# Kernel optimization log

Measured on AMD Instinct MI355X. Metric: run time of the kernel, lower is better.

The kernel has to match this reference:

```python
import jax, jax.numpy as jnp
import numpy as np

HEADS = 16
NUM_LANDMARKS = 64
PINV_ITERS = 6
D_MODEL = 1024


def _moore_penrose_pinv(x, num_iters):
    # Newton-Schulz iteration: V <- 0.25*V @ (13I - KV @ (15I - KV @ (7I - KV)))
    m = x.shape[-1]
    I = jnp.eye(m, dtype=x.dtype)
    V = x
    for _ in range(num_iters):
        KV = x @ V  # [..., m, m]
        V = 0.25 * V @ (13.0 * I - KV @ (15.0 * I - KV @ (7.0 * I - KV)))
    return V


def setup_inputs() -> dict:
    key = jax.random.key(0)
    k1, k2, k3 = jax.random.split(key, 3)
    b, n, d = 4, 4096, D_MODEL
    hidden_states = jax.random.normal(k1, (b, n, d), dtype=jnp.float32)
    Wqkv = jax.random.normal(k2, (d, 3 * d), dtype=jnp.float32) * 0.02
    bqkv = jnp.zeros((3 * d,), dtype=jnp.float32)
    Wout = jax.random.normal(k3, (d, d), dtype=jnp.float32) * 0.02
    bout = jnp.zeros((d,), dtype=jnp.float32)
    return {"hidden_states": hidden_states, "Wqkv": Wqkv, "bqkv": bqkv,
            "Wout": Wout, "bout": bout}


def reference(hidden_states, Wqkv, bqkv, Wout, bout):
    b, n, d = hidden_states.shape
    h, m = HEADS, NUM_LANDMARKS
    dh = d // h
    scale = 1.0 / np.sqrt(dh).astype(np.float32)
    # n is a multiple of m by construction, so the torch padding branch is a no-op.
    l = n // m  # tokens per landmark group

    qkv = hidden_states @ Wqkv + bqkv  # [b, n, 3d]
    q, k, v = jnp.split(qkv, 3, axis=-1)

    def to_heads(t):  # [b, n, d] -> [b, h, n, dh]
        return t.reshape(b, n, h, dh).transpose(0, 2, 1, 3)

    q, k, v = to_heads(q), to_heads(k), to_heads(v)
    q = q * scale

    # Landmarks: mean over contiguous groups of l tokens (sum / l in original).
    q_l = q.reshape(b, h, m, l, dh).mean(axis=3)  # [b, h, m, dh]
    k_l = k.reshape(b, h, m, l, dh).mean(axis=3)

    sim1 = jnp.einsum('bhid,bhjd->bhij', q, k_l)    # [b, h, n, m]
    sim2 = jnp.einsum('bhid,bhjd->bhij', q_l, k_l)  # [b, h, m, m]
    sim3 = jnp.einsum('bhid,bhjd->bhij', q_l, k)    # [b, h, m, n]

    attn1 = jax.nn.softmax(sim1, axis=-1)
    attn2 = jax.nn.softmax(sim2, axis=-1)
    attn3 = jax.nn.softmax(sim3, axis=-1)

    attn2_inv = _moore_penrose_pinv(attn2, PINV_ITERS)

    # out = attn1 @ attn2_inv @ (attn3 @ v), cheapest association
    out = attn1 @ (attn2_inv @ (attn3 @ v))  # [b, h, n, dh]
    out = out.transpose(0, 2, 1, 3).reshape(b, n, d)
    out = out @ Wout + bout
    return out
```

## Files before the change

### kernel.cpp

```cpp
#include <hip/hip_runtime.h>
#include <cstdint>

typedef unsigned short u16;
typedef __attribute__((ext_vector_type(8))) short s16x8;
typedef __attribute__((ext_vector_type(4))) float f32x4;

#define NTOK 4096
#define DH   64
#define DM   1024
#define NH   16

static __device__ __forceinline__ float b2f(u16 u){ return __uint_as_float(((unsigned)u)<<16); }
static __device__ __forceinline__ u16 f2b(float f){
  unsigned u = __float_as_uint(f);
  return (u16)((u + 0x7FFFu + ((u>>16)&1u)) >> 16);
}

static __device__ __forceinline__ void gload_lds16(const void* g, void* l) {
  __builtin_amdgcn_global_load_lds(
      (const __attribute__((address_space(1))) unsigned*)(uintptr_t)g,
      (__attribute__((address_space(3))) unsigned*)(uintptr_t)l, 16, 0, 0);
}

static __device__ __forceinline__ s16x8 ld8(const u16* p){ return *(const s16x8*)(const void*)p; }

__global__ __launch_bounds__(256) void k_cvt(const float* __restrict__ in, u16* __restrict__ out, long n4) {
  long i = (long)blockIdx.x*blockDim.x + threadIdx.x;
  const long st = (long)gridDim.x*blockDim.x;
  for (; i < n4; i += st) {
    const float4 v = ((const float4*)in)[i];
    ushort4 o; o.x=f2b(v.x); o.y=f2b(v.y); o.z=f2b(v.z); o.w=f2b(v.w);
    ((ushort4*)out)[i] = o;
  }
}

__global__ __launch_bounds__(256) void k_cvt_t(const float* __restrict__ in, u16* __restrict__ out, int R, int C) {
  __shared__ float tile[64][65];
  const int tc = blockIdx.x, tr = blockIdx.y;
  const int t = threadIdx.x, cx = t & 63, ry = t >> 6;
  #pragma unroll
  for (int p = 0; p < 16; ++p) {
    const int row = p*4 + ry;
    tile[row][cx] = in[(long)(tr*64 + row)*C + tc*64 + cx];
  }
  __syncthreads();
  #pragma unroll
  for (int p = 0; p < 16; ++p) {
    const int orow = p*4 + ry;
    out[(long)(tc*64 + orow)*R + tr*64 + cx] = f2b(tile[cx][orow]);
  }
}

__global__ __launch_bounds__(256) void k_xlmean(const float* __restrict__ hs, float* __restrict__ Xl) {
  const int row = blockIdx.x;
  const int b = row >> 6, lm = row & 63;
  const int d = blockIdx.y*256 + threadIdx.x;
  const float* p = hs + ((long)b*NTOK + lm*64)*DM + d;
  float s = 0.f;
  #pragma unroll 16
  for (int i = 0; i < 64; ++i) s += p[(long)i*DM];
  Xl[(long)row*DM + d] = s * (1.0f/64.0f);
}

__global__ __launch_bounds__(256) void k_lproj2(const float* __restrict__ Xl, const float* __restrict__ Wqkv,
                                                float* __restrict__ psum) {
  __shared__ __align__(16) float Xs[32][68];
  const int t = threadIdx.x;
  const int wcol = blockIdx.x*256 + t;
  const int r0 = blockIdx.y*32;
  const int kbase = blockIdx.z*128;
  float acc[32];
  #pragma unroll
  for (int r = 0; r < 32; ++r) acc[r] = 0.f;
  for (int k0 = kbase; k0 < kbase + 128; k0 += 64) {
    __syncthreads();
    for (int idx = t; idx < 2048; idx += 256)
      Xs[idx>>6][idx&63] = Xl[(long)(r0 + (idx>>6))*DM + k0 + (idx&63)];
    __syncthreads();
    for (int kk = 0; kk < 64; kk += 4) {
      f32x4 wv;
      #pragma unroll
      for (int j = 0; j < 4; ++j) wv[j] = Wqkv[(long)(k0+kk+j)*3072 + wcol];
      #pragma unroll
      for (int r = 0; r < 32; ++r) {
        const f32x4 xv = *(const f32x4*)&Xs[r][kk];
        acc[r] += xv[0]*wv[0] + xv[1]*wv[1] + xv[2]*wv[2] + xv[3]*wv[3];
      }
    }
  }
  float* po = psum + ((long)blockIdx.z*256 + r0)*2048 + wcol;
  #pragma unroll
  for (int r = 0; r < 32; ++r) po[(long)r*2048] = acc[r];
}

__global__ __launch_bounds__(256) void k_lreduce(const float* __restrict__ psum, const float* __restrict__ bqkv,
                                                 float* __restrict__ qlf, float* __restrict__ klf,
                                                 u16* __restrict__ qlb, u16* __restrict__ klb) {
  const long idx = (long)blockIdx.x*256 + threadIdx.x;
  const int row = (int)(idx >> 11), col = (int)(idx & 2047);
  float s = 0.f;
  #pragma unroll
  for (int z = 0; z < 8; ++z) s += psum[((long)z*256 + row)*2048 + col];
  const int isq = (col < 1024) ? 1 : 0;
  float val = s + bqkv[col];
  if (isq) val *= 0.125f;
  const int b = row >> 6, lm = row & 63;
  const int c2 = col & 1023, h = c2 >> 6, dh = c2 & 63;
  const long o = (((long)b*NH + h)*64 + lm)*64 + dh;
  if (isq) { qlf[o] = val; qlb[o] = f2b(val); }
  else     { klf[o] = val; klb[o] = f2b(val); }
}

template<int EPI>
__global__ __launch_bounds__(512, 2) void k_gemm256(
    const u16* __restrict__ A, const u16* __restrict__ Bt, const float* __restrict__ bias,
    int N, float* __restrict__ outF, u16* __restrict__ outQ, u16* __restrict__ outK, u16* __restrict__ outV)
{
  __shared__ __align__(16) u16 lds[4*16384];
  const int K = 1024;
  const int t = threadIdx.x;
  const int lane = t & 63;
  const int wid = t >> 6;
  const int c = lane & 15, g = lane >> 4;
  const int wm = wid >> 2, wn = wid & 3;
  const long arow0 = (long)blockIdx.x * 256;
  const long brow0 = (long)blockIdx.y * 256;
  char* ldsb = (char*)lds;

  const int srow = t >> 2;
  const int schunk = (t & 3) ^ ((srow >> 1) & 3);
  const u16* gA0 = A  + (arow0 + srow)*K       + schunk*8;
  const u16* gA1 = A  + (arow0 + 128 + srow)*K + schunk*8;
  const u16* gB0 = Bt + (brow0 + srow)*K       + schunk*8;
  const u16* gB1 = Bt + (brow0 + 128 + srow)*K + schunk*8;
  const int dstoff = t*16;

#define STAGE_A(kt) { char* bse = ldsb + ((kt)&3)*32768; \
    gload_lds16(gA0 + (kt)*32, bse + dstoff); \
    gload_lds16(gA1 + (kt)*32, bse + 8192 + dstoff); }
#define STAGE_B(kt) { char* bse = ldsb + ((kt)&3)*32768 + 16384; \
    gload_lds16(gB0 + (kt)*32, bse + dstoff); \
    gload_lds16(gB1 + (kt)*32, bse + 8192 + dstoff); }

  const int gs = g ^ ((c >> 1) & 3);
  int aoff[2][4], boff[4];
  #pragma unroll
  for (int mi = 0; mi < 4; ++mi) {
    aoff[0][mi] = (0*128 + wm*64 + mi*16 + c)*64 + gs*16;
    aoff[1][mi] = (1*128 + wm*64 + mi*16 + c)*64 + gs*16;
    boff[mi]    = 16384 + (wn*64 + mi*16 + c)*64 + gs*16;
  }

  f32x4 acc0[4][4] = {};
  f32x4 acc1[4][4] = {};

  STAGE_A(0); STAGE_B(0); STAGE_A(1); STAGE_B(1); STAGE_A(2); STAGE_B(2);
  asm volatile("s_waitcnt vmcnt(8)" ::: "memory");
  __builtin_amdgcn_s_barrier();

  for (int kt = 0; kt < 32; ++kt) {
    char* buf = ldsb + (kt&3)*32768;
    if (kt + 3 < 32) { STAGE_A(kt+3) STAGE_B(kt+3) }
    s16x8 af[4], af2[4], bfr[4];
    #pragma unroll
    for (int mi = 0; mi < 4; ++mi) af[mi]  = *(const s16x8*)(buf + aoff[0][mi]);
    #pragma unroll
    for (int ni = 0; ni < 4; ++ni) bfr[ni] = *(const s16x8*)(buf + boff[ni]);
    #pragma unroll
    for (int mi = 0; mi < 4; ++mi) af2[mi] = *(const s16x8*)(buf + aoff[1][mi]);
    asm volatile("s_waitcnt lgkmcnt(0)" ::: "memory");
    __builtin_amdgcn_sched_barrier(0);
    __builtin_amdgcn_s_setprio(1);
    #pragma unroll
    for (int mi = 0; mi < 4; ++mi)
      #pragma unroll
      for (int ni = 0; ni < 4; ++ni)
        acc0[mi][ni] = __builtin_amdgcn_mfma_f32_16x16x32_bf16(af[mi], bfr[ni], acc0[mi][ni], 0, 0, 0);
    #pragma unroll
    for (int mi = 0; mi < 4; ++mi)
      #pragma unroll
      for (int ni = 0; ni < 4; ++ni)
        acc1[mi][ni] = __builtin_amdgcn_mfma_f32_16x16x32_bf16(af2[mi], bfr[ni], acc1[mi][ni], 0, 0, 0);
    __builtin_amdgcn_s_setprio(0);
    if (kt <= 28)      { asm volatile("s_waitcnt vmcnt(8)" ::: "memory"); }
    else if (kt == 29) { asm volatile("s_waitcnt vmcnt(4)" ::: "memory"); }
    else if (kt == 30) { asm volatile("s_waitcnt vmcnt(0)" ::: "memory"); }
    __builtin_amdgcn_s_barrier();
  }
#undef STAGE_A
#undef STAGE_B

  if (EPI == 0) {
    const int tensor = (int)(brow0 >> 10);
    u16* dst = (tensor == 0) ? outQ : (tensor == 1) ? outK : outV;
    const float mul = (tensor == 0) ? 0.125f : 1.0f;
    #pragma unroll
    for (int ph = 0; ph < 2; ++ph)
      #pragma unroll
      for (int mi = 0; mi < 4; ++mi) {
        const int rowb = ph*128 + wm*64 + mi*16 + g*4;
        #pragma unroll
        for (int ni = 0; ni < 4; ++ni) {
          const long gcol = brow0 + wn*64 + ni*16 + c;
          const int c2 = (int)(gcol & 1023);
          const int head = c2 >> 6, dh = c2 & 63;
          const float bv = bias[gcol];
          const f32x4 a = ph ? acc1[mi][ni] : acc0[mi][ni];
          #pragma unroll
          for (int r = 0; r < 4; ++r) {
            const long grow = arow0 + rowb + r;
            const int b = (int)(grow >> 12), tok = (int)(grow & 4095);
            dst[(((long)b*NH + head)*NTOK + tok)*DH + dh] = f2b((a[r] + bv)*mul);
          }
        }
      }
  } else {
    #pragma unroll
    for (int ph = 0; ph < 2; ++ph)
      #pragma unroll
      for (int mi = 0; mi < 4; ++mi) {
        const int rowb = ph*128 + wm*64 + mi*16 + g*4;
        #pragma unroll
        for (int ni = 0; ni < 4; ++ni) {
          const long gcol = brow0 + wn*64 + ni*16 + c;
          const float bv = bias[gcol];
          const f32x4 a = ph ? acc1[mi][ni] : acc0[mi][ni];
          #pragma unroll
          for (int r = 0; r < 4; ++r) {
            const long grow = arow0 + rowb + r;
            outF[grow*N + gcol] = a[r] + bv;
          }
        }
      }
  }
}

__global__ __launch_bounds__(256) void k_vtrans(const u16* __restrict__ v, u16* __restrict__ vt) {
  __shared__ u16 tile[64][65];
  const int bh = blockIdx.x >> 6, tt = blockIdx.x & 63;
  const int t = threadIdx.x, cx = t & 63, ry = t >> 6;
  const u16* vp = v + ((long)bh*NTOK + tt*64)*DH;
  #pragma unroll
  for (int p = 0; p < 16; ++p) { const int row = p*4 + ry; tile[row][cx] = vp[row*DH + cx]; }
  __syncthreads();
  u16* op = vt + (long)bh*DH*NTOK + tt*64;
  #pragma unroll
  for (int p = 0; p < 16; ++p) { const int orow = p*4 + ry; op[(long)orow*NTOK + cx] = tile[cx][orow]; }
}

#define PST 68
static __device__ __forceinline__ void mm_nn8(const float* A, const float* B, float* C, int t) {
  const int lane = t & 63, j0 = (t >> 6) << 3;
  float acc[8];
  #pragma unroll
  for (int j = 0; j < 8; ++j) acc[j] = 0.f;
  for (int k = 0; k < 64; k += 4) {
    const f32x4 a4 = *(const f32x4*)&A[lane*PST + k];
    #pragma unroll
    for (int dk = 0; dk < 4; ++dk) {
      const float a = a4[dk];
      const float* br = &B[(k + dk)*PST + j0];
      const f32x4 b0 = *(const f32x4*)(br);
      const f32x4 b1 = *(const f32x4*)(br + 4);
      #pragma unroll
      for (int qq = 0; qq < 4; ++qq) { acc[qq] += a*b0[qq]; acc[4+qq] += a*b1[qq]; }
    }
  }
  #pragma unroll
  for (int j = 0; j < 8; ++j) C[lane*PST + j0 + j] = acc[j];
}
static __device__ __forceinline__ void mm_nt8(const float* A, const float* B, float* C, int t) {
  const int lane = t & 63, j0 = (t >> 6) << 3;
  float acc[8];
  #pragma unroll
  for (int j = 0; j < 8; ++j) acc[j] = 0.f;
  for (int k = 0; k < 64; k += 4) {
    const f32x4 a4 = *(const f32x4*)&A[lane*PST + k];
    #pragma unroll
    for (int jj = 0; jj < 8; ++jj) {
      const f32x4 b4 = *(const f32x4*)&B[(j0 + jj)*PST + k];
      acc[jj] += a4[0]*b4[0] + a4[1]*b4[1] + a4[2]*b4[2] + a4[3]*b4[3];
    }
  }
  #pragma unroll
  for (int j = 0; j < 8; ++j) C[lane*PST + j0 + j] = acc[j];
}

__global__ __launch_bounds__(512) void k_pinv(const float* __restrict__ qlf, const float* __restrict__ klf,
                                              float* __restrict__ a2inv) {
  __shared__ __align__(16) float Xb[64*PST];
  __shared__ __align__(16) float Vb[64*PST];
  __shared__ __align__(16) float T1[64*PST];
  __shared__ __align__(16) float T2[64*PST];
  __shared__ __align__(16) float T3[64*PST];
  const int bh = blockIdx.x, t = threadIdx.x;
  const float* ql = qlf + (long)bh*4096;
  const float* kl = klf + (long)bh*4096;
  for (int i = t; i < 4096; i += 512) { T1[(i>>6)*PST + (i&63)] = ql[i]; T2[(i>>6)*PST + (i&63)] = kl[i]; }
  __syncthreads();
  mm_nt8(T1, T2, Xb, t);
  __syncthreads();
  if (t < 64) {
    float mx = -1e30f;
    for (int j = 0; j < 64; ++j) mx = fmaxf(mx, Xb[t*PST + j]);
    float s = 0.f;
    for (int j = 0; j < 64; ++j) { const float e = expf(Xb[t*PST + j] - mx); Xb[t*PST + j] = e; s += e; }
    const float inv = 1.0f/s;
    for (int j = 0; j < 64; ++j) Xb[t*PST + j] *= inv;
  }
  __syncthreads();
  for (int i = t; i < 4096; i += 512) { const int r = i>>6, cc = i&63; Vb[r*PST+cc] = Xb[r*PST+cc]; }
  __syncthreads();
  for (int it = 0; it < 6; ++it) {
    mm_nn8(Xb, Vb, T1, t);  __syncthreads();
    for (int i = t; i < 4096; i += 512) { const int r=i>>6, cc=i&63; T2[r*PST+cc] = (r==cc?7.0f:0.0f) - T1[r*PST+cc]; }
    __syncthreads();
    mm_nn8(T1, T2, T3, t);  __syncthreads();
    for (int i = t; i < 4096; i += 512) { const int r=i>>6, cc=i&63; T2[r*PST+cc] = (r==cc?15.0f:0.0f) - T3[r*PST+cc]; }
    __syncthreads();
    mm_nn8(T1, T2, T3, t);  __syncthreads();
    for (int i = t; i < 4096; i += 512) { const int r=i>>6, cc=i&63; T2[r*PST+cc] = (r==cc?13.0f:0.0f) - T3[r*PST+cc]; }
    __syncthreads();
    mm_nn8(Vb, T2, T3, t);  __syncthreads();
    for (int i = t; i < 4096; i += 512) { const int r=i>>6, cc=i&63; Vb[r*PST+cc] = 0.25f*T3[r*PST+cc]; }
    __syncthreads();
  }
  for (int i = t; i < 4096; i += 512) a2inv[(long)bh*4096 + i] = Vb[(i>>6)*PST + (i&63)];
}

__global__ __launch_bounds__(256) void k_attn3v_p(const u16* __restrict__ qlb, const u16* __restrict__ kk,
                                                  const u16* __restrict__ vt,
                                                  float* __restrict__ zp, float* __restrict__ sp) {
  __shared__ __align__(16) float Zl[4][64][64];
  __shared__ float Sl[4][64];
  __shared__ __align__(16) u16 Pl[4][64][40];
  const int bh = blockIdx.x >> 2, qt = blockIdx.x & 3;
  const int t = threadIdx.x, w = t >> 6, lane = t & 63;
  const int c = lane & 15, g = lane >> 4;

  s16x8 aq[4][2];
  const u16* qlp = qlb + (long)bh*4096;
  #pragma unroll
  for (int mi = 0; mi < 4; ++mi)
    #pragma unroll
    for (int ks = 0; ks < 2; ++ks)
      aq[mi][ks] = ld8(qlp + (mi*16 + c)*64 + ks*32 + g*8);

  f32x4 zacc[4][4] = {};
  float sl[4][4] = {};
  const u16* kp = kk + (long)bh*NTOK*DH;
  const u16* vp = vt + (long)bh*DH*NTOK;
  char* pbase = (char*)&Pl[w][0][0];
  const int tok00 = qt*1024 + w*256;

  for (int it = 0; it < 8; ++it) {
    const int t0 = tok00 + it*32;
    f32x4 sacc[4][2] = {};
    s16x8 kb[2][2];
    #pragma unroll
    for (int cg = 0; cg < 2; ++cg)
      #pragma unroll
      for (int ks = 0; ks < 2; ++ks)
        kb[cg][ks] = ld8(kp + (long)(t0 + cg*16 + c)*64 + ks*32 + g*8);
    #pragma unroll
    for (int cg = 0; cg < 2; ++cg)
      #pragma unroll
      for (int ks = 0; ks < 2; ++ks)
        #pragma unroll
        for (int mi = 0; mi < 4; ++mi)
          sacc[mi][cg] = __builtin_amdgcn_mfma_f32_16x16x32_bf16(aq[mi][ks], kb[cg][ks], sacc[mi][cg], 0, 0, 0);
    #pragma unroll
    for (int mi = 0; mi < 4; ++mi)
      #pragma unroll
      for (int r = 0; r < 4; ++r) {
        const int row = mi*16 + g*4 + r;
        const float p0 = __expf(sacc[mi][0][r]);
        const float p1 = __expf(sacc[mi][1][r]);
        sl[mi][r] += p0 + p1;
        char* base = pbase + row*80;
        *(u16*)(base + c*2)      = f2b(p0);
        *(u16*)(base + 32 + c*2) = f2b(p1);
      }
    s16x8 pa[4];
    #pragma unroll
    for (int mi = 0; mi < 4; ++mi) pa[mi] = *(const s16x8*)(pbase + (mi*16 + c)*80 + g*16);
    #pragma unroll
    for (int ni = 0; ni < 4; ++ni) {
      const s16x8 vb = ld8(vp + (long)(ni*16 + c)*NTOK + t0 + g*8);
      #pragma unroll
      for (int mi = 0; mi < 4; ++mi)
        zacc[mi][ni] = __builtin_amdgcn_mfma_f32_16x16x32_bf16(pa[mi], vb, zacc[mi][ni], 0, 0, 0);
    }
  }
  #pragma unroll
  for (int mi = 0; mi < 4; ++mi)
    #pragma unroll
    for (int r = 0; r < 4; ++r) {
      float s = sl[mi][r];
      s += __shfl_xor(s, 1); s += __shfl_xor(s, 2); s += __shfl_xor(s, 4); s += __shfl_xor(s, 8);
      sl[mi][r] = s;
    }
  #pragma unroll
  for (int mi = 0; mi < 4; ++mi)
    #pragma unroll
    for (int ni = 0; ni < 4; ++ni)
      #pragma unroll
      for (int r = 0; r < 4; ++r)
        Zl[w][mi*16 + g*4 + r][ni*16 + c] = zacc[mi][ni][r];
  if (c == 0)
    #pragma unroll
    for (int mi = 0; mi < 4; ++mi)
      #pragma unroll
      for (int r = 0; r < 4; ++r)
        Sl[w][mi*16 + g*4 + r] = sl[mi][r];
  __syncthreads();
  float* zpp = zp + (long)blockIdx.x*4096;
  for (int i = t; i < 4096; i += 256) {
    const int row = i >> 6, dh = i & 63;
    zpp[i] = Zl[0][row][dh] + Zl[1][row][dh] + Zl[2][row][dh] + Zl[3][row][dh];
  }
  if (t < 64) sp[(long)blockIdx.x*64 + t] = Sl[0][t] + Sl[1][t] + Sl[2][t] + Sl[3][t];
}

__global__ __launch_bounds__(256) void k_zred(const float* __restrict__ zp, const float* __restrict__ sp,
                                              float* __restrict__ z) {
  const int bh = blockIdx.x, t = threadIdx.x;
  for (int i = t; i < 4096; i += 256) {
    const int row = i >> 6;
    float zs = 0.f, ss = 0.f;
    #pragma unroll
    for (int qt = 0; qt < 4; ++qt) {
      zs += zp[((long)(bh*4 + qt))*4096 + i];
      ss += sp[(long)(bh*4 + qt)*64 + row];
    }
    z[(long)bh*4096 + i] = zs / ss;
  }
}

__global__ __launch_bounds__(512) void k_w2(const float* __restrict__ a2inv, const float* __restrict__ z,
                                            u16* __restrict__ w2t) {
  __shared__ __align__(16) float Ai[64*PST];
  __shared__ __align__(16) float Zi[64*PST];
  __shared__ __align__(16) float Ci[64*PST];
  const int bh = blockIdx.x, t = threadIdx.x;
  for (int i = t; i < 4096; i += 512) {
    Ai[(i>>6)*PST + (i&63)] = a2inv[(long)bh*4096 + i];
    Zi[(i>>6)*PST + (i&63)] = z[(long)bh*4096 + i];
  }
  __syncthreads();
  mm_nn8(Ai, Zi, Ci, t);
  __syncthreads();
  for (int i = t; i < 4096; i += 512) { const int r = i>>6, cc = i&63; w2t[(long)bh*4096 + cc*64 + r] = f2b(Ci[r*PST + cc]); }
}

#define P1ST 144
__global__ __launch_bounds__(256) void k_attn1(const u16* __restrict__ q, const u16* __restrict__ klb,
                                               const u16* __restrict__ w2t, u16* __restrict__ ao) {
  __shared__ __align__(16) u16 Pl[4][64][72];
  const int bx = blockIdx.x, bh = bx >> 4, tt = bx & 15;
  const int b = bh >> 4, h = bh & 15;
  const int t = threadIdx.x, w = t >> 6, lane = t & 63;
  const int c = lane & 15, g = lane >> 4;
  const int tok0 = tt*256 + w*64;
  const u16* qp  = q + ((long)bh*NTOK + tok0)*DH;
  const u16* klp = klb + (long)bh*4096;
  const u16* wp  = w2t + (long)bh*4096;
  char* pbase = (char*)&Pl[w][0][0];

  s16x8 aq[4][2], kb[4][2], wb[4][2];
  #pragma unroll
  for (int i = 0; i < 4; ++i)
    #pragma unroll
    for (int ks = 0; ks < 2; ++ks) {
      aq[i][ks] = ld8(qp + (long)(i*16 + c)*DH + ks*32 + g*8);
      kb[i][ks] = ld8(klp + (i*16 + c)*64 + ks*32 + g*8);
      wb[i][ks] = ld8(wp  + (i*16 + c)*64 + ks*32 + g*8);
    }
  f32x4 sacc[4][4] = {};
  #pragma unroll
  for (int ks = 0; ks < 2; ++ks)
    #pragma unroll
    for (int mi = 0; mi < 4; ++mi)
      #pragma unroll
      for (int ni = 0; ni < 4; ++ni)
        sacc[mi][ni] = __builtin_amdgcn_mfma_f32_16x16x32_bf16(aq[mi][ks], kb[ni][ks], sacc[mi][ni], 0, 0, 0);

  float rs[4][4];
  #pragma unroll
  for (int mi = 0; mi < 4; ++mi)
    #pragma unroll
    for (int r = 0; r < 4; ++r) {
      const int row = mi*16 + g*4 + r;
      char* base = pbase + row*P1ST;
      float ssum = 0.f;
      #pragma unroll
      for (int ni = 0; ni < 4; ++ni) {
        const float p = __expf(sacc[mi][ni][r]);
        ssum += p;
        *(u16*)(base + (ni*16 + c)*2) = f2b(p);
      }
      ssum += __shfl_xor(ssum, 1); ssum += __shfl_xor(ssum, 2);
      ssum += __shfl_xor(ssum, 4); ssum += __shfl_xor(ssum, 8);
      rs[mi][r] = ssum;
    }
  __builtin_amdgcn_s_barrier();
  s16x8 pa[4][2];
  #pragma unroll
  for (int mi = 0; mi < 4; ++mi)
    #pragma unroll
    for (int ks = 0; ks < 2; ++ks)
      pa[mi][ks] = *(const s16x8*)(pbase + (mi*16 + c)*P1ST + ks*64 + g*16);
  f32x4 oacc[4][4] = {};
  #pragma unroll
  for (int ks = 0; ks < 2; ++ks)
    #pragma unroll
    for (int mi = 0; mi < 4; ++mi)
      #pragma unroll
      for (int ni = 0; ni < 4; ++ni)
        oacc[mi][ni] = __builtin_amdgcn_mfma_f32_16x16x32_bf16(pa[mi][ks], wb[ni][ks], oacc[mi][ni], 0, 0, 0);

  u16* op = ao + (long)b*NTOK*DM + (long)h*64;
  #pragma unroll
  for (int mi = 0; mi < 4; ++mi)
    #pragma unroll
    for (int r = 0; r < 4; ++r) {
      const int tok = tok0 + mi*16 + g*4 + r;
      const float inv = 1.0f / rs[mi][r];
      #pragma unroll
      for (int ni = 0; ni < 4; ++ni)
        op[(long)tok*DM + ni*16 + c] = f2b(oacc[mi][ni][r] * inv);
    }
}

extern "C" void kernel_launch(void* const* d_in, const int* in_sizes, int n_in,
                              void* d_out, int out_size, void* d_ws, size_t ws_size,
                              hipStream_t stream) {
  const float* hs   = (const float*)d_in[0];
  const float* Wqkv = (const float*)d_in[1];
  const float* bqkv = (const float*)d_in[2];
  const float* Wout = (const float*)d_in[3];
  const float* bout = (const float*)d_in[4];
  float* out = (float*)d_out;
  char* w = (char*)d_ws;

  u16*  Xb    = (u16*)(w);
  float* zp   = (float*)(w);
  float* sp   = (float*)(w + 4194304L);
  u16*  WqkvT = (u16*)(w + 33554432L);
  u16*  WoutT = (u16*)(w + 39845888L);
  u16*  q     = (u16*)(w + 41943040L);
  float* psum = (float*)(w + 41943040L);
  u16*  k     = (u16*)(w + 75497472L);
  u16*  v     = (u16*)(w + 109051904L);
  u16*  vt    = (u16*)(w + 142606336L);
  float* Xl   = (float*)(w + 142606336L);
  float* qlf  = (float*)(w + 176160768L);
  float* klf  = (float*)(w + 177209344L);
  u16*  qlb   = (u16*)(w + 178257920L);
  u16*  klb   = (u16*)(w + 178782208L);
  float* a2i  = (float*)(w + 179306496L);
  float* z    = (float*)(w + 180355072L);
  u16*  w2t   = (u16*)(w + 181403648L);
  u16*  ao    = (u16*)(w + 181927936L);

  k_cvt<<<2048, 256, 0, stream>>>(hs, Xb, 4194304L);
  k_cvt_t<<<dim3(48,16), 256, 0, stream>>>(Wqkv, WqkvT, 1024, 3072);
  k_cvt_t<<<dim3(16,16), 256, 0, stream>>>(Wout, WoutT, 1024, 1024);
  k_xlmean<<<dim3(256,4), 256, 0, stream>>>(hs, Xl);
  k_lproj2<<<dim3(8,8,8), 256, 0, stream>>>(Xl, Wqkv, psum);
  k_lreduce<<<2048, 256, 0, stream>>>(psum, bqkv, qlf, klf, qlb, klb);
  k_gemm256<0><<<dim3(64,12), 512, 0, stream>>>(Xb, WqkvT, bqkv, 3072, nullptr, q, k, v);
  k_vtrans<<<4096, 256, 0, stream>>>(v, vt);
  k_pinv<<<64, 512, 0, stream>>>(qlf, klf, a2i);
  k_attn3v_p<<<256, 256, 0, stream>>>(qlb, k, vt, zp, sp);
  k_zred<<<64, 256, 0, stream>>>(zp, sp, z);
  k_w2<<<64, 512, 0, stream>>>(a2i, z, w2t);
  k_attn1<<<1024, 256, 0, stream>>>(q, klb, w2t, ao);
  k_gemm256<1><<<dim3(64,4), 512, 0, stream>>>(ao, WoutT, bout, 1024, out, nullptr, nullptr, nullptr);
}
```

Measured before the change: 374.9 us.

## Fuse bf16 conversion with landmark mean and software-pipeline LDS fragment loads in GEMM

Merges the hidden-state fp32-to-bf16 conversion and the landmark-mean reduction into one kernel, so the 64MB input is read once instead of twice. Separately restructures the GEMM main loop so the next k-tile's A/B fragments are loaded from LDS during the second half of the MFMA work, and the second A fragment load overlaps the first MFMA batch. The aim is to hide LDS latency behind MFMA execution. This adds register pressure from the extra fragment buffers and depends on a more delicate ordering of barriers and waitcnts.

```diff
diff --git a/kernel.cpp b/kernel.cpp
--- a/kernel.cpp
+++ b/kernel.cpp
@@ -24,14 +24,20 @@
 
 static __device__ __forceinline__ s16x8 ld8(const u16* p){ return *(const s16x8*)(const void*)p; }
 
-__global__ __launch_bounds__(256) void k_cvt(const float* __restrict__ in, u16* __restrict__ out, long n4) {
-  long i = (long)blockIdx.x*blockDim.x + threadIdx.x;
-  const long st = (long)gridDim.x*blockDim.x;
-  for (; i < n4; i += st) {
-    const float4 v = ((const float4*)in)[i];
-    ushort4 o; o.x=f2b(v.x); o.y=f2b(v.y); o.z=f2b(v.z); o.w=f2b(v.w);
-    ((ushort4*)out)[i] = o;
-  }
+__global__ __launch_bounds__(256) void k_cvt_xl(const float* __restrict__ hs, u16* __restrict__ Xb,
+                                                float* __restrict__ Xl) {
+  const int grp = blockIdx.x;
+  const int d = blockIdx.y*256 + threadIdx.x;
+  const float* p = hs + (long)grp*64*DM + d;
+  u16* xo = Xb + (long)grp*64*DM + d;
+  float s = 0.f;
+  #pragma unroll 8
+  for (int i = 0; i < 64; ++i) {
+    const float v = p[(long)i*DM];
+    s += v;
+    xo[(long)i*DM] = f2b(v);
+  }
+  Xl[(long)grp*DM + d] = s * (1.0f/64.0f);
 }
 
 __global__ __launch_bounds__(256) void k_cvt_t(const float* __restrict__ in, u16* __restrict__ out, int R, int C) {
@@ -49,17 +55,6 @@
     const int orow = p*4 + ry;
     out[(long)(tc*64 + orow)*R + tr*64 + cx] = f2b(tile[cx][orow]);
   }
-}
-
-__global__ __launch_bounds__(256) void k_xlmean(const float* __restrict__ hs, float* __restrict__ Xl) {
-  const int row = blockIdx.x;
-  const int b = row >> 6, lm = row & 63;
-  const int d = blockIdx.y*256 + threadIdx.x;
-  const float* p = hs + ((long)b*NTOK + lm*64)*DM + d;
-  float s = 0.f;
-  #pragma unroll 16
-  for (int i = 0; i < 64; ++i) s += p[(long)i*DM];
-  Xl[(long)row*DM + d] = s * (1.0f/64.0f);
 }
 
 __global__ __launch_bounds__(256) void k_lproj2(const float* __restrict__ Xl, const float* __restrict__ Wqkv,
@@ -158,34 +153,53 @@
   asm volatile("s_waitcnt vmcnt(8)" ::: "memory");
   __builtin_amdgcn_s_barrier();
 
+  s16x8 af[4], bfr[4], af2[4];
+  #pragma unroll
+  for (int mi = 0; mi < 4; ++mi) af[mi]  = *(const s16x8*)(ldsb + aoff[0][mi]);
+  #pragma unroll
+  for (int ni = 0; ni < 4; ++ni) bfr[ni] = *(const s16x8*)(ldsb + boff[ni]);
+
   for (int kt = 0; kt < 32; ++kt) {
-    char* buf = ldsb + (kt&3)*32768;
+    char* buf  = ldsb + (kt&3)*32768;
+    char* bufn = ldsb + ((kt+1)&3)*32768;
     if (kt + 3 < 32) { STAGE_A(kt+3) STAGE_B(kt+3) }
-    s16x8 af[4], af2[4], bfr[4];
-    #pragma unroll
-    for (int mi = 0; mi < 4; ++mi) af[mi]  = *(const s16x8*)(buf + aoff[0][mi]);
-    #pragma unroll
-    for (int ni = 0; ni < 4; ++ni) bfr[ni] = *(const s16x8*)(buf + boff[ni]);
-    #pragma unroll
-    for (int mi = 0; mi < 4; ++mi) af2[mi] = *(const s16x8*)(buf + aoff[1][mi]);
     asm volatile("s_waitcnt lgkmcnt(0)" ::: "memory");
     __builtin_amdgcn_sched_barrier(0);
+    #pragma unroll
+    for (int mi = 0; mi < 4; ++mi) af2[mi] = *(const s16x8*)(buf + aoff[1][mi]);
+    __builtin_amdgcn_sched_barrier(0);
     __builtin_amdgcn_s_setprio(1);
     #pragma unroll
     for (int mi = 0; mi < 4; ++mi)
       #pragma unroll
       for (int ni = 0; ni < 4; ++ni)
         acc0[mi][ni] = __builtin_amdgcn_mfma_f32_16x16x32_bf16(af[mi], bfr[ni], acc0[mi][ni], 0, 0, 0);
+    __builtin_amdgcn_s_setprio(0);
+    asm volatile("s_waitcnt lgkmcnt(0)" ::: "memory");
+    __builtin_amdgcn_sched_barrier(0);
+    if (kt <= 28)      { asm volatile("s_waitcnt vmcnt(8)" ::: "memory"); }
+    else if (kt == 29) { asm volatile("s_waitcnt vmcnt(4)" ::: "memory"); }
+    else if (kt == 30) { asm volatile("s_waitcnt vmcnt(0)" ::: "memory"); }
+    if (kt < 31) __builtin_amdgcn_s_barrier();
+    s16x8 nf[4], nb[4];
+    if (kt < 31) {
+      #pragma unroll
+      for (int mi = 0; mi < 4; ++mi) nf[mi] = *(const s16x8*)(bufn + aoff[0][mi]);
+      #pragma unroll
+      for (int ni = 0; ni < 4; ++ni) nb[ni] = *(const s16x8*)(bufn + boff[ni]);
+    }
+    __builtin_amdgcn_sched_barrier(0);
+    __builtin_amdgcn_s_setprio(1);
     #pragma unroll
     for (int mi = 0; mi < 4; ++mi)
       #pragma unroll
       for (int ni = 0; ni < 4; ++ni)
         acc1[mi][ni] = __builtin_amdgcn_mfma_f32_16x16x32_bf16(af2[mi], bfr[ni], acc1[mi][ni], 0, 0, 0);
     __builtin_amdgcn_s_setprio(0);
-    if (kt <= 28)      { asm volatile("s_waitcnt vmcnt(8)" ::: "memory"); }
-    else if (kt == 29) { asm volatile("s_waitcnt vmcnt(4)" ::: "memory"); }
-    else if (kt == 30) { asm volatile("s_waitcnt vmcnt(0)" ::: "memory"); }
-    __builtin_amdgcn_s_barrier();
+    if (kt < 31) {
+      #pragma unroll
+      for (int mi = 0; mi < 4; ++mi) { af[mi] = nf[mi]; bfr[mi] = nb[mi]; }
+    }
   }
 #undef STAGE_A
 #undef STAGE_B
@@ -563,10 +577,9 @@
   u16*  w2t   = (u16*)(w + 181403648L);
   u16*  ao    = (u16*)(w + 181927936L);
 
-  k_cvt<<<2048, 256, 0, stream>>>(hs, Xb, 4194304L);
+  k_cvt_xl<<<dim3(256,4), 256, 0, stream>>>(hs, Xb, Xl);
   k_cvt_t<<<dim3(48,16), 256, 0, stream>>>(Wqkv, WqkvT, 1024, 3072);
   k_cvt_t<<<dim3(16,16), 256, 0, stream>>>(Wout, WoutT, 1024, 1024);
-  k_xlmean<<<dim3(256,4), 256, 0, stream>>>(hs, Xl);
   k_lproj2<<<dim3(8,8,8), 256, 0, stream>>>(Xl, Wqkv, psum);
   k_lreduce<<<2048, 256, 0, stream>>>(psum, bqkv, qlf, klf, qlb, klb);
   k_gemm256<0><<<dim3(64,12), 512, 0, stream>>>(Xb, WqkvT, bqkv, 3072, nullptr, q, k, v);
```

Result: faster. 364.6 us (-2.7%).
